# Kernel tuning notes

Hardware: AMD Instinct MI355X
Metric: run time of the kernel (lower is better)

## Reference

```python
import jax, jax.numpy as jnp
import numpy as np

N = 5000          # nodes (pool_ratios = [2000/5000, 0.5])
KS = (2000, 1000, 500)  # top-k sizes per level, depth=3
H = 128           # inter_dim
IN = 3            # xyz
OUT = 6890        # SMPL template vertices
E = 80000


def _gcn(adj, x, W, b):
    # GCNConv: add self-loops (weight 1), symmetric normalization
    n = adj.shape[0]
    A = adj + jnp.eye(n, dtype=adj.dtype)
    dinv = jax.lax.rsqrt(A.sum(axis=1))
    Ahat = dinv[:, None] * A * dinv[None, :]
    return Ahat @ (x @ W) + b


def _augment(adj):
    # GraphUNet.augment_adj: remove self loops, add self loops, A @ A, remove self loops
    n = adj.shape[0]
    eye = jnp.eye(n, dtype=adj.dtype)
    A = adj * (1.0 - eye) + eye
    A2 = A @ A
    return A2 * (1.0 - eye)


def _pool(x, adj, w, k):
    # TopKPooling: score = tanh(x.w / ||w||), keep top-k, scale kept features by score
    score = jnp.tanh((x @ w) / jnp.linalg.norm(w))
    sc, perm = jax.lax.top_k(score, k)
    x = x[perm] * sc[:, None]
    adj = adj[perm][:, perm]
    return x, adj, perm


def reference(pos, edge_index, Wd0, bd0, Wd1, bd1, Wd2, bd2, Wd3, bd3,
              pw0, pw1, pw2, Wu0, bu0, Wu1, bu1, Wu2, bu2,
              W1, b1, W2, b2, W3, b3):
    # eval mode: dropout_adj(p=0.1, training=False) is identity
    adj = jnp.zeros((N, N), pos.dtype).at[edge_index[0], edge_index[1]].add(1.0)

    x = jax.nn.relu(_gcn(adj, pos, Wd0, bd0))
    xs, adjs, perms = [x], [adj], []
    Wds = [(Wd1, bd1), (Wd2, bd2), (Wd3, bd3)]
    pws = [pw0, pw1, pw2]

    adj_cur = adj
    for i in range(3):
        a = _augment(adj_cur)
        x, adj_cur, perm = _pool(x, a, pws[i], KS[i])
        Wi, bi = Wds[i]
        x = jax.nn.relu(_gcn(adj_cur, x, Wi, bi))
        if i < 2:
            xs.append(x)
            adjs.append(adj_cur)
        perms.append(perm)

    Wus = [(Wu0, bu0), (Wu1, bu1), (Wu2, bu2)]
    for i in range(3):
        j = 2 - i
        res = xs[j]
        up = jnp.zeros_like(res).at[perms[j]].set(x)  # unpool: scatter back
        x = res + up                                   # sum_res=True
        Wi, bi = Wus[i]
        x = _gcn(adjs[j], x, Wi, bi)
        if i < 2:
            x = jax.nn.relu(x)

    x = x @ W1 + b1
    x = jax.nn.relu(x) @ W2 + b2
    x = x @ W3 + b3
    return jax.nn.log_softmax(x, axis=1)


def _glorot(k, shape):
    return (jax.random.normal(k, shape) * np.sqrt(2.0 / (shape[0] + shape[1]))).astype(jnp.float32)


def setup_inputs() -> dict:
    key = jax.random.key(0)
    ks = jax.random.split(key, 16)
    inp = {
        'pos': jax.random.normal(ks[0], (N, IN), dtype=jnp.float32),
        'edge_index': jax.random.randint(ks[1], (2, E), 0, N, dtype=jnp.int64),
        'Wd0': _glorot(ks[2], (IN, H)), 'bd0': jnp.zeros((H,), jnp.float32),
        'Wd1': _glorot(ks[3], (H, H)), 'bd1': jnp.zeros((H,), jnp.float32),
        'Wd2': _glorot(ks[4], (H, H)), 'bd2': jnp.zeros((H,), jnp.float32),
        'Wd3': _glorot(ks[5], (H, H)), 'bd3': jnp.zeros((H,), jnp.float32),
        'pw0': jax.random.normal(ks[6], (H,), dtype=jnp.float32) / np.sqrt(H),
        'pw1': jax.random.normal(ks[7], (H,), dtype=jnp.float32) / np.sqrt(H),
        'pw2': jax.random.normal(ks[8], (H,), dtype=jnp.float32) / np.sqrt(H),
        'Wu0': _glorot(ks[9], (H, H)), 'bu0': jnp.zeros((H,), jnp.float32),
        'Wu1': _glorot(ks[10], (H, H)), 'bu1': jnp.zeros((H,), jnp.float32),
        'Wu2': _glorot(ks[11], (H, H)), 'bu2': jnp.zeros((H,), jnp.float32),
        'W1': _glorot(ks[12], (H, H)), 'b1': jnp.zeros((H,), jnp.float32),
        'W2': _glorot(ks[13], (H, H)), 'b2': jnp.zeros((H,), jnp.float32),
        'W3': _glorot(ks[14], (H, OUT)), 'b3': jnp.zeros((OUT,), jnp.float32),
    }
    return inp
```

## Files before the change

### kernel.cpp

```cpp
#include <hip/hip_runtime.h>
#include <cmath>

#define CDIV(a,b) (((a)+(b)-1)/(b))

using u16 = unsigned short;
using short8 = __attribute__((ext_vector_type(8))) short;
using f32x4 = __attribute__((ext_vector_type(4))) float;

__device__ __forceinline__ u16 f2b(float v) {
    union { float f; unsigned u; } x; x.f = v;
    unsigned r = x.u + 0x7fffu + ((x.u >> 16) & 1u);
    return (u16)(r >> 16);
}
__device__ __forceinline__ float b2f(u16 h) {
    union { unsigned u; float f; } x; x.u = ((unsigned)h) << 16;
    return x.f;
}

#if defined(__has_builtin)
#if __has_builtin(__builtin_amdgcn_global_load_lds)
#define HAS_GLL 1
#endif
#endif
#ifndef HAS_GLL
#define HAS_GLL 0
#endif

__device__ __forceinline__ void g2l(const u16* g, uint4* l) {
#if HAS_GLL
    __builtin_amdgcn_global_load_lds((const __attribute__((address_space(1))) void*)g,
                                     (__attribute__((address_space(3))) void*)l, 16, 0, 0);
#else
    *l = *(const uint4*)g;
#endif
}


__global__ void build_adj_k(const int* __restrict__ ei, float* __restrict__ adj, int E, int ld) {
    int e = blockIdx.x * 256 + threadIdx.x;
    if (e < E) {
        int s = ei[e];
        int d = ei[E + e];
        atomicAdd(&adj[(size_t)s * ld + d], 1.0f);
    }
}

__global__ void rowsum_dinv_b_k(const u16* __restrict__ adjb, int ld, int n, float* __restrict__ dinv) {
    int i = blockIdx.x;
    __shared__ float red[256];
    const u16* row = adjb + (size_t)i * ld;
    float s = 0.f;
    for (int j = threadIdx.x; j < n; j += 256) s += b2f(row[j]);
    red[threadIdx.x] = s; __syncthreads();
    for (int w = 128; w > 0; w >>= 1) {
        if (threadIdx.x < w) red[threadIdx.x] += red[threadIdx.x + w];
        __syncthreads();
    }
    if (threadIdx.x == 0) dinv[i] = rsqrtf(red[0] + 1.0f);
}

__global__ void convS_k(const float* __restrict__ in, u16* __restrict__ out, size_t n4) {
    size_t i = (size_t)blockIdx.x * 256 + threadIdx.x;
    if (i < n4) {
        float4 v = ((const float4*)in)[i];
        ushort4 o;
        o.x = f2b(v.x); o.y = f2b(v.y); o.z = f2b(v.z); o.w = f2b(v.w);
        ((ushort4*)out)[i] = o;
    }
}

__global__ void transpose_b_k(const u16* __restrict__ in, u16* __restrict__ out, int n) {
    __shared__ u16 t[64][65];
    int i0 = blockIdx.y * 64, j0 = blockIdx.x * 64;
    for (int e = threadIdx.x; e < 4096; e += 256) {
        int r = e >> 6, c = e & 63;
        t[r][c] = in[(size_t)(i0 + r) * n + j0 + c];
    }
    __syncthreads();
    for (int e = threadIdx.x; e < 4096; e += 256) {
        int r = e >> 6, c = e & 63;
        out[(size_t)(j0 + r) * n + i0 + c] = t[c][r];
    }
}


__global__ void csr_cnt_k(const int* __restrict__ ei, int E, int* __restrict__ rowcnt) {
    int e = blockIdx.x * 256 + threadIdx.x;
    if (e < E) {
        int u = ei[e], v = ei[E + e];
        if (u != v) atomicAdd(&rowcnt[u], 1);
    }
}

__global__ __launch_bounds__(1024) void prefix_k(const int* __restrict__ cnt, int* __restrict__ ptr, int n) {
    __shared__ int buf[5120];
    for (int i = threadIdx.x; i < 5120; i += 1024) buf[i] = (i < n) ? cnt[i] : 0;
    __syncthreads();
    for (int d = 1; d < 5120; d <<= 1) {
        int vals[5];
#pragma unroll
        for (int c = 0; c < 5; ++c) {
            int i = threadIdx.x + c * 1024;
            vals[c] = (i >= d) ? buf[i - d] : 0;
        }
        __syncthreads();
#pragma unroll
        for (int c = 0; c < 5; ++c) {
            int i = threadIdx.x + c * 1024;
            buf[i] += vals[c];
        }
        __syncthreads();
    }
    for (int i = threadIdx.x; i <= n; i += 1024) ptr[i] = (i == 0) ? 0 : buf[i - 1];
}

__global__ void csr_fill_k(const int* __restrict__ ei, int E, const int* __restrict__ rowptr,
                           int* __restrict__ fill, int* __restrict__ cols) {
    int e = blockIdx.x * 256 + threadIdx.x;
    if (e < E) {
        int u = ei[e], v = ei[E + e];
        if (u != v) {
            int p = rowptr[u] + atomicAdd(&fill[u], 1);
            cols[p] = v;
        }
    }
}

__global__ void inv_k(const int* __restrict__ perm, int k, int* __restrict__ inv) {
    int r = blockIdx.x * 256 + threadIdx.x;
    if (r < k) inv[perm[r]] = r;
}

__global__ __launch_bounds__(256) void spgemm_k(const int* __restrict__ perm, const int* __restrict__ rowptr,
                                                const int* __restrict__ cols, const int* __restrict__ inv,
                                                int* __restrict__ A2, int ldo) {
    __shared__ int nb[256];
    __shared__ int degs;
    int a = blockIdx.x;
    int pa = perm[a];
    int s = rowptr[pa], epos = rowptr[pa + 1];
    int d = epos - s;
    if (threadIdx.x == 0) degs = d > 256 ? 256 : d;
    if (threadIdx.x < d && threadIdx.x < 256) nb[threadIdx.x] = cols[s + threadIdx.x];
    __syncthreads();
    int* rowA2 = A2 + (size_t)a * ldo;
    for (int p = s + threadIdx.x; p < epos; p += 256) {
        int b = inv[cols[p]];
        if (b >= 0) atomicAdd(&rowA2[b], 2);
    }
    int dd = degs;
    for (int j = 0; j < dd; ++j) {
        int kk = nb[j];
        int s2 = rowptr[kk], e2 = rowptr[kk + 1];
        for (int p = s2 + threadIdx.x; p < e2; p += 256) {
            int b = inv[cols[p]];
            if (b >= 0) atomicAdd(&rowA2[b], 1);
        }
    }
}

__global__ void conv_spg_k(const int* __restrict__ A2, int kNew, int Mp, u16* __restrict__ out) {
    int r = blockIdx.x;
    for (int j = threadIdx.x; j < Mp; j += 256) {
        int v = 0;
        if (r < kNew && j < kNew && j != r) v = A2[(size_t)r * Mp + j];
        out[(size_t)r * Mp + j] = f2b((float)v);
    }
}


template<int SA, int SB>
__global__ __launch_bounds__(256) void mm_nt(const u16* __restrict__ A0, const u16* __restrict__ A1,
                                             const u16* __restrict__ B0, const u16* __restrict__ B1,
                                             float* __restrict__ C, const float* __restrict__ cbias,
                                             int M, int N, int lda, int ldb, int ldc,
                                             int kPerZ, int Kpad, size_t cstride) {
    __shared__ uint4 lds_t[(2 + SA + SB) * 512];
    uint4* Ab  = lds_t;
    uint4* A1b = lds_t + (SA ? 512 : 0);
    uint4* Bb  = lds_t + (1 + SA) * 512;
    uint4* B1b = Bb + (SB ? 512 : 0);

    int tid = threadIdx.x;

    int nx = gridDim.x, nxy = nx * gridDim.y;
    int bx = blockIdx.x, by = blockIdx.y;
    if ((nxy & 7) == 0) {
        int flat = by * nx + bx;
        int nf = (flat & 7) * (nxy >> 3) + (flat >> 3);
        bx = nf % nx; by = nf / nx;
    }
    int row0 = by * 128, col0 = bx * 128;

    int kbeg = blockIdx.z * kPerZ;
    int kend = min(kbeg + kPerZ, Kpad);
    C += (size_t)blockIdx.z * cstride;

    int wave = tid >> 6, lane = tid & 63;
    int wr = (wave >> 1) * 64, wc = (wave & 1) * 64;
    int lrow = lane & 15, kg = lane >> 4;

    int tS0 = tid, tS1 = tid + 256;
    int R0 = ((tS0 >> 6) << 4) | (tS0 & 15), kc0 = (tS0 >> 4) & 3;
    int R1 = ((tS1 >> 6) << 4) | (tS1 & 15), kc1 = (tS1 >> 4) & 3;

    const u16* aP0 = A0 + (size_t)(row0 + R0) * lda + kbeg + kc0 * 8;
    const u16* aP1 = A0 + (size_t)(row0 + R1) * lda + kbeg + kc1 * 8;
    const u16* bP0 = B0 + (size_t)(col0 + R0) * ldb + kbeg + kc0 * 8;
    const u16* bP1 = B0 + (size_t)(col0 + R1) * ldb + kbeg + kc1 * 8;
    const u16* a1P0 = SA ? (A1 + (size_t)(row0 + R0) * lda + kbeg + kc0 * 8) : nullptr;
    const u16* a1P1 = SA ? (A1 + (size_t)(row0 + R1) * lda + kbeg + kc1 * 8) : nullptr;
    const u16* b1P0 = SB ? (B1 + (size_t)(col0 + R0) * ldb + kbeg + kc0 * 8) : nullptr;
    const u16* b1P1 = SB ? (B1 + (size_t)(col0 + R1) * ldb + kbeg + kc1 * 8) : nullptr;

    f32x4 acc[4][4] = {};

    for (int k0 = kbeg; k0 < kend; k0 += 32) {
        __syncthreads();
        g2l(aP0, Ab + tS0);
        g2l(aP1, Ab + tS1);
        if constexpr (SA) { g2l(a1P0, A1b + tS0); g2l(a1P1, A1b + tS1); }
        g2l(bP0, Bb + tS0);
        g2l(bP1, Bb + tS1);
        if constexpr (SB) { g2l(b1P0, B1b + tS0); g2l(b1P1, B1b + tS1); }
        __syncthreads();

        const short8* Ap  = (const short8*)Ab;
        const short8* A1p = (const short8*)A1b;
        const short8* Bp  = (const short8*)Bb;
        const short8* B1p = (const short8*)B1b;

        short8 a[4], a1[4], b[4], b1[4];
#pragma unroll
        for (int m = 0; m < 4; ++m) {
            int idx = (((wr >> 4) + m) << 6) | (kg << 4) | lrow;
            a[m] = Ap[idx];
            if constexpr (SA) a1[m] = A1p[idx];
        }
#pragma unroll
        for (int n = 0; n < 4; ++n) {
            int idx = (((wc >> 4) + n) << 6) | (kg << 4) | lrow;
            b[n] = Bp[idx];
            if constexpr (SB) b1[n] = B1p[idx];
        }
#pragma unroll
        for (int m = 0; m < 4; ++m)
#pragma unroll
            for (int n = 0; n < 4; ++n) {
                acc[m][n] = __builtin_amdgcn_mfma_f32_16x16x32_bf16(a[m], b[n], acc[m][n], 0, 0, 0);
                if constexpr (SA) acc[m][n] = __builtin_amdgcn_mfma_f32_16x16x32_bf16(a1[m], b[n], acc[m][n], 0, 0, 0);
                if constexpr (SB) acc[m][n] = __builtin_amdgcn_mfma_f32_16x16x32_bf16(a[m], b1[n], acc[m][n], 0, 0, 0);
            }

        aP0 += 32; aP1 += 32; bP0 += 32; bP1 += 32;
        if constexpr (SA) { a1P0 += 32; a1P1 += 32; }
        if constexpr (SB) { b1P0 += 32; b1P1 += 32; }
    }

#pragma unroll
    for (int m = 0; m < 4; ++m) {
        int rm = row0 + wr + m * 16 + kg * 4;
#pragma unroll
        for (int n = 0; n < 4; ++n) {
            int cc = col0 + wc + n * 16 + lrow;
            if (cc >= N) continue;
            float badd = cbias ? cbias[cc] : 0.f;
#pragma unroll
            for (int i = 0; i < 4; ++i) {
                int r = rm + i;
                if (r < M) C[(size_t)r * ldc + cc] = acc[m][n][i] + badd;
            }
        }
    }
}


__global__ __launch_bounds__(256) void gemm64(const float* __restrict__ A, const float* __restrict__ B,
                                              float* __restrict__ C,
                                              int M, int N, int K, int lda, int ldb, int ldc,
                                              const float* __restrict__ bias, int relu) {
    __shared__ float As[16][65];
    __shared__ float Bs[16][65];
    int tid = threadIdx.x;
    int trow = tid / 16, tcol = tid % 16;
    int row0 = blockIdx.y * 64 + trow * 4;
    int col0 = blockIdx.x * 64 + tcol * 4;
    float acc[4][4] = {};
    int am = tid >> 2;
    int ak = (tid & 3) * 4;
    int bk = tid >> 4;
    int bn = (tid & 15) * 4;
    for (int k0 = 0; k0 < K; k0 += 16) {
        int gm = blockIdx.y * 64 + am;
#pragma unroll
        for (int u = 0; u < 4; ++u) {
            int gk = k0 + ak + u;
            As[ak + u][am] = (gm < M && gk < K) ? A[(size_t)gm * lda + gk] : 0.f;
        }
        int gbk = k0 + bk;
#pragma unroll
        for (int u = 0; u < 4; ++u) {
            int gn = blockIdx.x * 64 + bn + u;
            Bs[bk][bn + u] = (gbk < K && gn < N) ? B[(size_t)gbk * ldb + gn] : 0.f;
        }
        __syncthreads();
#pragma unroll
        for (int kk = 0; kk < 16; ++kk) {
            float a[4], b[4];
#pragma unroll
            for (int i = 0; i < 4; ++i) a[i] = As[kk][trow * 4 + i];
#pragma unroll
            for (int j = 0; j < 4; ++j) b[j] = Bs[kk][tcol * 4 + j];
#pragma unroll
            for (int i = 0; i < 4; ++i)
#pragma unroll
                for (int j = 0; j < 4; ++j) acc[i][j] += a[i] * b[j];
        }
        __syncthreads();
    }
#pragma unroll
    for (int i = 0; i < 4; ++i) {
        int r = row0 + i;
        if (r >= M) continue;
#pragma unroll
        for (int j = 0; j < 4; ++j) {
            int c = col0 + j;
            if (c < N) {
                float v = acc[i][j] + (bias ? bias[c] : 0.f);
                if (relu) v = fmaxf(v, 0.f);
                C[(size_t)r * ldc + c] = v;
            }
        }
    }
}


__global__ void scale_split_k(const float* __restrict__ xw, const float* __restrict__ dinv,
                              u16* __restrict__ zhT, u16* __restrict__ zlT, int M, int ldz) {
    __shared__ float t[32][33];
    int i0 = blockIdx.x * 32, f0 = blockIdx.y * 32;
#pragma unroll
    for (int it = 0; it < 4; ++it) {
        int r = it * 8 + (threadIdx.x >> 5);
        int c = threadIdx.x & 31;
        int i = i0 + r;
        t[r][c] = (i < M) ? dinv[i] * xw[(size_t)i * 128 + f0 + c] : 0.f;
    }
    __syncthreads();
#pragma unroll
    for (int it = 0; it < 4; ++it) {
        int r = it * 8 + (threadIdx.x >> 5);
        int c = threadIdx.x & 31;
        int f = f0 + r, i = i0 + c;
        float v = t[c][r];
        u16 h = f2b(v);
        zhT[(size_t)f * ldz + i] = h;
        zlT[(size_t)f * ldz + i] = f2b(v - b2f(h));
    }
}

__global__ void reduce_gcn_post_k(const float* __restrict__ part, int Z, int Mp,
                                  const float* __restrict__ xw, const float* __restrict__ dinv,
                                  const float* __restrict__ bias, float* __restrict__ y, int relu) {
    int i = blockIdx.x, f = threadIdx.x;
    size_t idx = (size_t)i * 128 + f;
    float s = 0.f;
    for (int z = 0; z < Z; ++z) s += part[(size_t)z * Mp * 128 + idx];
    float di = dinv[i];
    float v = di * s + di * di * xw[idx] + bias[f];
    y[idx] = relu ? fmaxf(v, 0.f) : v;
}


__global__ void score_k(const float* __restrict__ x, const float* __restrict__ pw,
                        float* __restrict__ score) {
    int i = blockIdx.x;
    __shared__ float red[128], red2[128];
    float p = pw[threadIdx.x];
    red[threadIdx.x]  = x[(size_t)i * 128 + threadIdx.x] * p;
    red2[threadIdx.x] = p * p;
    __syncthreads();
    for (int s = 64; s > 0; s >>= 1) {
        if (threadIdx.x < s) { red[threadIdx.x] += red[threadIdx.x + s]; red2[threadIdx.x] += red2[threadIdx.x + s]; }
        __syncthreads();
    }
    if (threadIdx.x == 0) score[i] = tanhf(red[0] / sqrtf(red2[0]));
}

__global__ __launch_bounds__(256) void rank_partial_k(const float* __restrict__ score, int n,
                                                      int* __restrict__ rankpart) {
    __shared__ float s_sh[512];
    int i = blockIdx.x * 256 + threadIdx.x;
    int jbase = blockIdx.y * 512;
    float si = (i < n) ? score[i] : -3.0f;
    for (int t = threadIdx.x; t < 512; t += 256) {
        int j = jbase + t;
        s_sh[t] = (j < n) ? score[j] : -3.0f;
    }
    __syncthreads();
    int cnt = 0;
#pragma unroll 16
    for (int t = 0; t < 512; ++t) {
        float sj = s_sh[t];
        cnt += (sj > si) || (sj == si && (jbase + t) < i);
    }
    if (i < n) rankpart[blockIdx.y * n + i] = cnt;
}

__global__ void scatter_topk_k(const float* __restrict__ score, const int* __restrict__ rankpart,
                               int nsl, int n, int k, int* __restrict__ perm, float* __restrict__ sc) {
    int i = blockIdx.x * 256 + threadIdx.x;
    if (i >= n) return;
    int r = 0;
    for (int s = 0; s < nsl; ++s) r += rankpart[s * n + i];
    if (r < k) { perm[r] = i; sc[r] = score[i]; }
}

__global__ void pool_x_k(float* __restrict__ xo, const float* __restrict__ xi,
                         const int* __restrict__ perm, const float* __restrict__ sc) {
    int a = blockIdx.x, f = threadIdx.x;
    xo[(size_t)a * 128 + f] = xi[(size_t)perm[a] * 128 + f] * sc[a];
}

__global__ void gather2_b_k(const u16* __restrict__ src0, const u16* __restrict__ src1,
                            int ldsrc, const int* __restrict__ perm,
                            u16* __restrict__ dst0, u16* __restrict__ dst1, int width) {
    const u16* src = blockIdx.y ? src1 : src0;
    u16* dst = blockIdx.y ? dst1 : dst0;
    int row = blockIdx.x;
    int p = perm[row];
    const uint4* s4 = (const uint4*)(src + (size_t)p * ldsrc);
    uint4* d4 = (uint4*)(dst + (size_t)row * width);
    int n8 = width >> 3;
    for (int j = threadIdx.x; j < n8; j += 256) d4[j] = s4[j];
    __syncthreads();
    if (threadIdx.x == 0) dst[(size_t)row * width + p] = 0x3F80;
}

__global__ void reduce_pool_k(const float* __restrict__ part, int Z, int k, int Mp, u16* __restrict__ out) {
    int row = blockIdx.x;
    for (int j = threadIdx.x; j < Mp; j += 256) {
        float s = 0.f;
        if (row < k && j < k) {
            for (int z = 0; z < Z; ++z) s += part[(size_t)z * Mp * Mp + (size_t)row * Mp + j];
            if (j == row) s = 0.f;
        }
        out[(size_t)row * Mp + j] = f2b(s);
    }
}

__global__ void scatter_add_k(float* __restrict__ xdst, const int* __restrict__ perm,
                              const float* __restrict__ xsrc) {
    int a = blockIdx.x, f = threadIdx.x;
    xdst[(size_t)perm[a] * 128 + f] += xsrc[(size_t)a * 128 + f];
}


__global__ void split_head_k(const float* __restrict__ x, u16* __restrict__ Ah, u16* __restrict__ Al) {
    int i = blockIdx.x, f = threadIdx.x;
    size_t idx = (size_t)i * 128 + f;
    float v = x[idx];
    u16 h = f2b(v);
    Ah[idx] = h;
    Al[idx] = f2b(v - b2f(h));
}

__global__ void convW3T_k(const float* __restrict__ W3, u16* __restrict__ W3T, int Nc, int Ncp) {
    __shared__ float t[64][65];
    int k0 = blockIdx.y * 64, n0 = blockIdx.x * 64;
    for (int e = threadIdx.x; e < 4096; e += 256) {
        int r = e >> 6, c = e & 63;
        t[r][c] = (k0 + r < 128 && n0 + c < Nc) ? W3[(size_t)(k0 + r) * Nc + n0 + c] : 0.f;
    }
    __syncthreads();
    for (int e = threadIdx.x; e < 4096; e += 256) {
        int r = e >> 6, c = e & 63;
        int nn = n0 + r, kk = k0 + c;
        if (nn < Ncp) W3T[(size_t)nn * 128 + kk] = f2b(t[c][r]);
    }
}

__global__ __launch_bounds__(256) void logsoftmax_k(float* __restrict__ out) {
    const int C = 6890;
    const int CPT = 27;
    int row = blockIdx.x;
    float* rowp = out + (size_t)row * C;
    __shared__ float red[256];

    float v[CPT];
    float mx = -1e30f;
#pragma unroll
    for (int u = 0; u < CPT; ++u) {
        int c = threadIdx.x + u * 256;
        v[u] = (c < C) ? rowp[c] : -1e30f;
        mx = fmaxf(mx, v[u]);
    }
    red[threadIdx.x] = mx; __syncthreads();
    for (int s = 128; s > 0; s >>= 1) {
        if (threadIdx.x < s) red[threadIdx.x] = fmaxf(red[threadIdx.x], red[threadIdx.x + s]);
        __syncthreads();
    }
    float m = red[0];
    __syncthreads();

    float sum = 0.f;
#pragma unroll
    for (int u = 0; u < CPT; ++u) sum += __expf(v[u] - m);
    red[threadIdx.x] = sum; __syncthreads();
    for (int s = 128; s > 0; s >>= 1) {
        if (threadIdx.x < s) red[threadIdx.x] += red[threadIdx.x + s];
        __syncthreads();
    }
    float ls = m + logf(red[0]);

#pragma unroll
    for (int u = 0; u < CPT; ++u) {
        int c = threadIdx.x + u * 256;
        if (c < C) rowp[c] = v[u] - ls;
    }
}


extern "C" void kernel_launch(void* const* d_in, const int* in_sizes, int n_in,
                              void* d_out, int out_size, void* d_ws, size_t ws_size,
                              hipStream_t stream) {
    const int N0 = 5000, K1 = 2000, K2 = 1000, K3 = 500, E = 80000, OUTC = 6890;
    const int Np0 = 5120, Kp1 = 2048, Kp2 = 1024, Kp3 = 512, OUTCP = 6912;
    (void)in_sizes; (void)n_in; (void)out_size; (void)ws_size;

    const float* pos = (const float*)d_in[0];
    const int*   ei  = (const int*)d_in[1];
    const float* Wd0 = (const float*)d_in[2];  const float* bd0 = (const float*)d_in[3];
    const float* Wd1 = (const float*)d_in[4];  const float* bd1 = (const float*)d_in[5];
    const float* Wd2 = (const float*)d_in[6];  const float* bd2 = (const float*)d_in[7];
    const float* Wd3 = (const float*)d_in[8];  const float* bd3 = (const float*)d_in[9];
    const float* pw0 = (const float*)d_in[10];
    const float* pw1 = (const float*)d_in[11];
    const float* pw2 = (const float*)d_in[12];
    const float* Wu0 = (const float*)d_in[13]; const float* bu0 = (const float*)d_in[14];
    const float* Wu1 = (const float*)d_in[15]; const float* bu1 = (const float*)d_in[16];
    const float* Wu2 = (const float*)d_in[17]; const float* bu2 = (const float*)d_in[18];
    const float* W1  = (const float*)d_in[19]; const float* b1  = (const float*)d_in[20];
    const float* W2  = (const float*)d_in[21]; const float* b2  = (const float*)d_in[22];
    const float* W3  = (const float*)d_in[23]; const float* b3  = (const float*)d_in[24];

    float* w = (float*)d_ws;
    size_t off = 0;
    auto alloc = [&](size_t nel) { float* p = w + off; off += nel; return p; };

    float* pool = alloc(26220000);
    float* adj0 = pool;
    float* partials = pool;
    u16* G   = (u16*)(pool + 13000000);
    u16* HT  = (u16*)(pool + 18250000);
    u16* zhT = (u16*)(pool + 13000000);
    u16* zlT = (u16*)(pool + 13400000);
    u16* Ah  = (u16*)(pool);
    u16* Al  = (u16*)(pool + 400000);

    u16* adj0b  = (u16*)alloc(13107200);
    u16* adj1b  = (u16*)alloc(2097152);
    u16* adj1bT = (u16*)alloc(2097152);
    u16* adj2b  = (u16*)alloc(524288);
    u16* adj2bT = (u16*)alloc(524288);
    u16* adj3b  = (u16*)alloc(131072);
    u16* W3T    = (u16*)alloc(442368);

    float* x0 = alloc((size_t)N0 * 128);
    float* x1 = alloc((size_t)K1 * 128);
    float* x2 = alloc((size_t)K2 * 128);
    float* xa = alloc((size_t)N0 * 128);
    float* xb = alloc((size_t)N0 * 128);
    float* xw = alloc((size_t)N0 * 128);
    float* dinv0 = alloc(N0); float* dinv1 = alloc(K1); float* dinv2 = alloc(K2); float* dinv3 = alloc(K3);
    float* scorev = alloc(N0);
    float* scv    = alloc(K1);
    int* perm0 = (int*)alloc(K1);
    int* perm1 = (int*)alloc(K2);
    int* perm2 = (int*)alloc(K3);
    int* rankpart = (int*)alloc(50048);
    int* rowcnt = (int*)alloc(5120);
    int* rowptr = (int*)alloc(5120);
    int* fillc  = (int*)alloc(5120);
    int* colsb  = (int*)alloc(80000);
    int* invb   = (int*)alloc(5120);

    auto launch_mm = [&](int SA, int SB, const u16* A0, const u16* A1, const u16* B0, const u16* B1,
                         float* Cc, const float* cbias, int M, int N, int Kpad,
                         int lda, int ldb, int ldc, size_t cstride, int Z) -> int {
        int kPerZ = CDIV(Kpad, Z * 32) * 32;
        int gz = CDIV(Kpad, kPerZ);
        dim3 g(CDIV(N, 128), CDIV(M, 128), gz);
        if (SA)      mm_nt<1, 0><<<g, 256, 0, stream>>>(A0, A1, B0, B1, Cc, cbias, M, N, lda, ldb, ldc, kPerZ, Kpad, cstride);
        else if (SB) mm_nt<0, 1><<<g, 256, 0, stream>>>(A0, A1, B0, B1, Cc, cbias, M, N, lda, ldb, ldc, kPerZ, Kpad, cstride);
        else         mm_nt<0, 0><<<g, 256, 0, stream>>>(A0, A1, B0, B1, Cc, cbias, M, N, lda, ldb, ldc, kPerZ, Kpad, cstride);
        return gz;
    };

    auto run_gcn = [&](const u16* adjb, int n, int Np,
                       const float* x, int kin, const float* W, const float* bias,
                       const float* dinv, int relu, float* y, int Z) {
        gemm64<<<dim3(2, CDIV(n, 64)), 256, 0, stream>>>(x, W, xw, n, 128, kin, kin, 128, 128, nullptr, 0);
        scale_split_k<<<dim3(Np / 32, 4), 256, 0, stream>>>(xw, dinv, zhT, zlT, n, Np);
        int gz = launch_mm(0, 1, adjb, nullptr, zhT, zlT, partials, nullptr,
                           Np, 128, Np, Np, Np, 128, (size_t)Np * 128, Z);
        reduce_gcn_post_k<<<n, 128, 0, stream>>>(partials, gz, Np, xw, dinv, bias, y, relu);
    };

    auto run_pool = [&](const float* x, int n, int Np, int kNew, int KpNew, const float* pw,
                        const u16* srcb, const u16* srcbT, u16* adjNew, int* perm, int Z) {
        score_k<<<n, 128, 0, stream>>>(x, pw, scorev);
        int nsl = CDIV(n, 512);
        rank_partial_k<<<dim3(CDIV(n, 256), nsl), 256, 0, stream>>>(scorev, n, rankpart);
        scatter_topk_k<<<CDIV(n, 256), 256, 0, stream>>>(scorev, rankpart, nsl, n, kNew, perm, scv);
        pool_x_k<<<kNew, 128, 0, stream>>>(xa, x, perm, scv);
        gather2_b_k<<<dim3(kNew, 2), 256, 0, stream>>>(srcb, srcbT, Np, perm, G, HT, Np);
        int gz = launch_mm(0, 0, G, nullptr, HT, nullptr, partials, nullptr,
                           KpNew, KpNew, Np, Np, Np, KpNew, (size_t)KpNew * KpNew, Z);
        reduce_pool_k<<<KpNew, 256, 0, stream>>>(partials, gz, kNew, KpNew, adjNew);
    };

    hipMemsetAsync(adj0, 0, (size_t)Np0 * Np0 * sizeof(float), stream);
    hipMemsetAsync(rowcnt, 0, N0 * sizeof(int), stream);
    hipMemsetAsync(fillc, 0, N0 * sizeof(int), stream);
    build_adj_k<<<CDIV(E, 256), 256, 0, stream>>>(ei, adj0, E, Np0);
    csr_cnt_k<<<CDIV(E, 256), 256, 0, stream>>>(ei, E, rowcnt);
    prefix_k<<<1, 1024, 0, stream>>>(rowcnt, rowptr, N0);
    csr_fill_k<<<CDIV(E, 256), 256, 0, stream>>>(ei, E, rowptr, fillc, colsb);
    convS_k<<<CDIV((size_t)Np0 * Np0 / 4, 256), 256, 0, stream>>>(adj0, adj0b, (size_t)Np0 * Np0 / 4);
    rowsum_dinv_b_k<<<N0, 256, 0, stream>>>(adj0b, Np0, Np0, dinv0);

    run_gcn(adj0b, N0, Np0, pos, 3, Wd0, bd0, dinv0, 1, x0, 10);

    score_k<<<N0, 128, 0, stream>>>(x0, pw0, scorev);
    {
        int nsl = CDIV(N0, 512);
        rank_partial_k<<<dim3(CDIV(N0, 256), nsl), 256, 0, stream>>>(scorev, N0, rankpart);
        scatter_topk_k<<<CDIV(N0, 256), 256, 0, stream>>>(scorev, rankpart, nsl, N0, K1, perm0, scv);
    }
    pool_x_k<<<K1, 128, 0, stream>>>(xa, x0, perm0, scv);
    hipMemsetAsync(invb, 0xFF, N0 * sizeof(int), stream);
    inv_k<<<CDIV(K1, 256), 256, 0, stream>>>(perm0, K1, invb);
    int* A2i = (int*)partials;
    hipMemsetAsync(A2i, 0, (size_t)Kp1 * Kp1 * sizeof(int), stream);
    spgemm_k<<<K1, 256, 0, stream>>>(perm0, rowptr, colsb, invb, A2i, Kp1);
    conv_spg_k<<<Kp1, 256, 0, stream>>>(A2i, K1, Kp1, adj1b);

    transpose_b_k<<<dim3(Kp1 / 64, Kp1 / 64), 256, 0, stream>>>(adj1b, adj1bT, Kp1);
    rowsum_dinv_b_k<<<K1, 256, 0, stream>>>(adj1b, Kp1, Kp1, dinv1);
    run_gcn(adj1b, K1, Kp1, xa, 128, Wd1, bd1, dinv1, 1, x1, 16);

    run_pool(x1, K1, Kp1, K2, Kp2, pw1, adj1b, adj1bT, adj2b, perm1, 8);
    transpose_b_k<<<dim3(Kp2 / 64, Kp2 / 64), 256, 0, stream>>>(adj2b, adj2bT, Kp2);
    rowsum_dinv_b_k<<<K2, 256, 0, stream>>>(adj2b, Kp2, Kp2, dinv2);
    run_gcn(adj2b, K2, Kp2, xa, 128, Wd2, bd2, dinv2, 1, x2, 16);

    run_pool(x2, K2, Kp2, K3, Kp3, pw2, adj2b, adj2bT, adj3b, perm2, 8);
    rowsum_dinv_b_k<<<K3, 256, 0, stream>>>(adj3b, Kp3, Kp3, dinv3);
    run_gcn(adj3b, K3, Kp3, xa, 128, Wd3, bd3, dinv3, 1, xb, 8);

    hipMemcpyAsync(xa, x2, (size_t)K2 * 128 * sizeof(float), hipMemcpyDeviceToDevice, stream);
    scatter_add_k<<<K3, 128, 0, stream>>>(xa, perm2, xb);
    run_gcn(adj2b, K2, Kp2, xa, 128, Wu0, bu0, dinv2, 1, xb, 16);

    hipMemcpyAsync(xa, x1, (size_t)K1 * 128 * sizeof(float), hipMemcpyDeviceToDevice, stream);
    scatter_add_k<<<K2, 128, 0, stream>>>(xa, perm1, xb);
    run_gcn(adj1b, K1, Kp1, xa, 128, Wu1, bu1, dinv1, 1, xb, 16);

    hipMemcpyAsync(xa, x0, (size_t)N0 * 128 * sizeof(float), hipMemcpyDeviceToDevice, stream);
    scatter_add_k<<<K1, 128, 0, stream>>>(xa, perm0, xb);
    run_gcn(adj0b, N0, Np0, xa, 128, Wu2, bu2, dinv0, 0, xb, 10);

    gemm64<<<dim3(2, CDIV(N0, 64)), 256, 0, stream>>>(xb, W1, xa, N0, 128, 128, 128, 128, 128, b1, 1);
    gemm64<<<dim3(2, CDIV(N0, 64)), 256, 0, stream>>>(xa, W2, xw, N0, 128, 128, 128, 128, 128, b2, 0);

    split_head_k<<<N0, 128, 0, stream>>>(xw, Ah, Al);
    convW3T_k<<<dim3(OUTCP / 64, 2), 256, 0, stream>>>(W3, W3T, OUTC, OUTCP);

    float* outp = (float*)d_out;
    launch_mm(1, 0, Ah, Al, W3T, nullptr, outp, b3, N0, OUTC, 128, 128, 128, OUTC, 0, 1);
    logsoftmax_k<<<N0, 256, 0, stream>>>(outp);
}
```

Measured before the change: 817.1 us.

## Replace dense level-0 adjacency GCN with sorted CSR sparse SpMM

Drops the dense 5120x5120 adjacency build, its bf16 conversion, the dense row-sum and the dense GEMM for the two level-0 GCN layers. Those now run as a CSR SpMM with degrees taken from the edge counts. Self-loop edges are now kept in the CSR and skipped inside the SpGEMM instead. Rows are insertion-sorted so the fp32 summation order is deterministic. This removes large memory traffic and a big dense matmul, in exchange for serial per-row sorting and a simple one-block-per-row SpMM.

```diff
diff --git a/kernel.cpp b/kernel.cpp
--- a/kernel.cpp
+++ b/kernel.cpp
@@ -36,60 +36,9 @@
 }
 
 
-__global__ void build_adj_k(const int* __restrict__ ei, float* __restrict__ adj, int E, int ld) {
-    int e = blockIdx.x * 256 + threadIdx.x;
-    if (e < E) {
-        int s = ei[e];
-        int d = ei[E + e];
-        atomicAdd(&adj[(size_t)s * ld + d], 1.0f);
-    }
-}
-
-__global__ void rowsum_dinv_b_k(const u16* __restrict__ adjb, int ld, int n, float* __restrict__ dinv) {
-    int i = blockIdx.x;
-    __shared__ float red[256];
-    const u16* row = adjb + (size_t)i * ld;
-    float s = 0.f;
-    for (int j = threadIdx.x; j < n; j += 256) s += b2f(row[j]);
-    red[threadIdx.x] = s; __syncthreads();
-    for (int w = 128; w > 0; w >>= 1) {
-        if (threadIdx.x < w) red[threadIdx.x] += red[threadIdx.x + w];
-        __syncthreads();
-    }
-    if (threadIdx.x == 0) dinv[i] = rsqrtf(red[0] + 1.0f);
-}
-
-__global__ void convS_k(const float* __restrict__ in, u16* __restrict__ out, size_t n4) {
-    size_t i = (size_t)blockIdx.x * 256 + threadIdx.x;
-    if (i < n4) {
-        float4 v = ((const float4*)in)[i];
-        ushort4 o;
-        o.x = f2b(v.x); o.y = f2b(v.y); o.z = f2b(v.z); o.w = f2b(v.w);
-        ((ushort4*)out)[i] = o;
-    }
-}
-
-__global__ void transpose_b_k(const u16* __restrict__ in, u16* __restrict__ out, int n) {
-    __shared__ u16 t[64][65];
-    int i0 = blockIdx.y * 64, j0 = blockIdx.x * 64;
-    for (int e = threadIdx.x; e < 4096; e += 256) {
-        int r = e >> 6, c = e & 63;
-        t[r][c] = in[(size_t)(i0 + r) * n + j0 + c];
-    }
-    __syncthreads();
-    for (int e = threadIdx.x; e < 4096; e += 256) {
-        int r = e >> 6, c = e & 63;
-        out[(size_t)(j0 + r) * n + i0 + c] = t[c][r];
-    }
-}
-
-
 __global__ void csr_cnt_k(const int* __restrict__ ei, int E, int* __restrict__ rowcnt) {
     int e = blockIdx.x * 256 + threadIdx.x;
-    if (e < E) {
-        int u = ei[e], v = ei[E + e];
-        if (u != v) atomicAdd(&rowcnt[u], 1);
-    }
+    if (e < E) atomicAdd(&rowcnt[ei[e]], 1);
 }
 
 __global__ __launch_bounds__(1024) void prefix_k(const int* __restrict__ cnt, int* __restrict__ ptr, int n) {
@@ -118,13 +67,44 @@
                            int* __restrict__ fill, int* __restrict__ cols) {
     int e = blockIdx.x * 256 + threadIdx.x;
     if (e < E) {
-        int u = ei[e], v = ei[E + e];
-        if (u != v) {
-            int p = rowptr[u] + atomicAdd(&fill[u], 1);
-            cols[p] = v;
-        }
-    }
-}
+        int u = ei[e];
+        int p = rowptr[u] + atomicAdd(&fill[u], 1);
+        cols[p] = ei[E + e];
+    }
+}
+
+__global__ void sortrows_k(const int* __restrict__ rowptr, int* __restrict__ cols, int n) {
+    int i = blockIdx.x * 256 + threadIdx.x;
+    if (i >= n) return;
+    int s = rowptr[i], e = rowptr[i + 1];
+    for (int p = s + 1; p < e; ++p) {
+        int v = cols[p];
+        int q = p - 1;
+        while (q >= s && cols[q] > v) { cols[q + 1] = cols[q]; --q; }
+        cols[q + 1] = v;
+    }
+}
+
+__global__ void dinv_from_cnt_k(const int* __restrict__ cnt, float* __restrict__ dinv, int n) {
+    int i = blockIdx.x * 256 + threadIdx.x;
+    if (i < n) dinv[i] = rsqrtf((float)cnt[i] + 1.0f);
+}
+
+__global__ __launch_bounds__(128) void spmm_gcn_k(const int* __restrict__ rowptr, const int* __restrict__ cols,
+                                                  const float* __restrict__ dinv, const float* __restrict__ xw,
+                                                  const float* __restrict__ bias, float* __restrict__ y, int relu) {
+    int i = blockIdx.x, f = threadIdx.x;
+    int s = rowptr[i], e = rowptr[i + 1];
+    float acc = 0.f;
+    for (int p = s; p < e; ++p) {
+        int d = cols[p];
+        acc += dinv[d] * xw[(size_t)d * 128 + f];
+    }
+    float di = dinv[i];
+    float v = di * acc + di * di * xw[(size_t)i * 128 + f] + bias[f];
+    y[(size_t)i * 128 + f] = relu ? fmaxf(v, 0.f) : v;
+}
+
 
 __global__ void inv_k(const int* __restrict__ perm, int k, int* __restrict__ inv) {
     int r = blockIdx.x * 256 + threadIdx.x;
@@ -145,16 +125,23 @@
     __syncthreads();
     int* rowA2 = A2 + (size_t)a * ldo;
     for (int p = s + threadIdx.x; p < epos; p += 256) {
-        int b = inv[cols[p]];
-        if (b >= 0) atomicAdd(&rowA2[b], 2);
+        int c = cols[p];
+        if (c != pa) {
+            int b = inv[c];
+            if (b >= 0) atomicAdd(&rowA2[b], 2);
+        }
     }
     int dd = degs;
     for (int j = 0; j < dd; ++j) {
         int kk = nb[j];
+        if (kk == pa) continue;
         int s2 = rowptr[kk], e2 = rowptr[kk + 1];
         for (int p = s2 + threadIdx.x; p < e2; p += 256) {
-            int b = inv[cols[p]];
-            if (b >= 0) atomicAdd(&rowA2[b], 1);
+            int pb = cols[p];
+            if (pb != kk) {
+                int b = inv[pb];
+                if (b >= 0) atomicAdd(&rowA2[b], 1);
+            }
         }
     }
 }
@@ -165,6 +152,35 @@
         int v = 0;
         if (r < kNew && j < kNew && j != r) v = A2[(size_t)r * Mp + j];
         out[(size_t)r * Mp + j] = f2b((float)v);
+    }
+}
+
+
+__global__ void rowsum_dinv_b_k(const u16* __restrict__ adjb, int ld, int n, float* __restrict__ dinv) {
+    int i = blockIdx.x;
+    __shared__ float red[256];
+    const u16* row = adjb + (size_t)i * ld;
+    float s = 0.f;
+    for (int j = threadIdx.x; j < n; j += 256) s += b2f(row[j]);
+    red[threadIdx.x] = s; __syncthreads();
+    for (int w = 128; w > 0; w >>= 1) {
+        if (threadIdx.x < w) red[threadIdx.x] += red[threadIdx.x + w];
+        __syncthreads();
+    }
+    if (threadIdx.x == 0) dinv[i] = rsqrtf(red[0] + 1.0f);
+}
+
+__global__ void transpose_b_k(const u16* __restrict__ in, u16* __restrict__ out, int n) {
+    __shared__ u16 t[64][65];
+    int i0 = blockIdx.y * 64, j0 = blockIdx.x * 64;
+    for (int e = threadIdx.x; e < 4096; e += 256) {
+        int r = e >> 6, c = e & 63;
+        t[r][c] = in[(size_t)(i0 + r) * n + j0 + c];
+    }
+    __syncthreads();
+    for (int e = threadIdx.x; e < 4096; e += 256) {
+        int r = e >> 6, c = e & 63;
+        out[(size_t)(j0 + r) * n + i0 + c] = t[c][r];
     }
 }
 
@@ -525,7 +541,7 @@
                               void* d_out, int out_size, void* d_ws, size_t ws_size,
                               hipStream_t stream) {
     const int N0 = 5000, K1 = 2000, K2 = 1000, K3 = 500, E = 80000, OUTC = 6890;
-    const int Np0 = 5120, Kp1 = 2048, Kp2 = 1024, Kp3 = 512, OUTCP = 6912;
+    const int Kp1 = 2048, Kp2 = 1024, Kp3 = 512, OUTCP = 6912;
     (void)in_sizes; (void)n_in; (void)out_size; (void)ws_size;
 
     const float* pos = (const float*)d_in[0];
@@ -549,7 +565,6 @@
     auto alloc = [&](size_t nel) { float* p = w + off; off += nel; return p; };
 
     float* pool = alloc(26220000);
-    float* adj0 = pool;
     float* partials = pool;
     u16* G   = (u16*)(pool + 13000000);
     u16* HT  = (u16*)(pool + 18250000);
@@ -558,7 +573,6 @@
     u16* Ah  = (u16*)(pool);
     u16* Al  = (u16*)(pool + 400000);
 
-    u16* adj0b  = (u16*)alloc(13107200);
     u16* adj1b  = (u16*)alloc(2097152);
     u16* adj1bT = (u16*)alloc(2097152);
     u16* adj2b  = (u16*)alloc(524288);
@@ -598,13 +612,18 @@
     };
 
     auto run_gcn = [&](const u16* adjb, int n, int Np,
-                       const float* x, int kin, const float* W, const float* bias,
+                       const float* x, const float* W, const float* bias,
                        const float* dinv, int relu, float* y, int Z) {
-        gemm64<<<dim3(2, CDIV(n, 64)), 256, 0, stream>>>(x, W, xw, n, 128, kin, kin, 128, 128, nullptr, 0);
+        gemm64<<<dim3(2, CDIV(n, 64)), 256, 0, stream>>>(x, W, xw, n, 128, 128, 128, 128, 128, nullptr, 0);
         scale_split_k<<<dim3(Np / 32, 4), 256, 0, stream>>>(xw, dinv, zhT, zlT, n, Np);
         int gz = launch_mm(0, 1, adjb, nullptr, zhT, zlT, partials, nullptr,
                            Np, 128, Np, Np, Np, 128, (size_t)Np * 128, Z);
         reduce_gcn_post_k<<<n, 128, 0, stream>>>(partials, gz, Np, xw, dinv, bias, y, relu);
+    };
+
+    auto run_gcn_sp = [&](const float* x, int kin, const float* W, const float* bias, int relu, float* y) {
+        gemm64<<<dim3(2, CDIV(N0, 64)), 256, 0, stream>>>(x, W, xw, N0, 128, kin, kin, 128, 128, nullptr, 0);
+        spmm_gcn_k<<<N0, 128, 0, stream>>>(rowptr, colsb, dinv0, xw, bias, y, relu);
     };
 
     auto run_pool = [&](const float* x, int n, int Np, int kNew, int KpNew, const float* pw,
@@ -620,17 +639,15 @@
         reduce_pool_k<<<KpNew, 256, 0, stream>>>(partials, gz, kNew, KpNew, adjNew);
     };
 
-    hipMemsetAsync(adj0, 0, (size_t)Np0 * Np0 * sizeof(float), stream);
     hipMemsetAsync(rowcnt, 0, N0 * sizeof(int), stream);
     hipMemsetAsync(fillc, 0, N0 * sizeof(int), stream);
-    build_adj_k<<<CDIV(E, 256), 256, 0, stream>>>(ei, adj0, E, Np0);
     csr_cnt_k<<<CDIV(E, 256), 256, 0, stream>>>(ei, E, rowcnt);
     prefix_k<<<1, 1024, 0, stream>>>(rowcnt, rowptr, N0);
     csr_fill_k<<<CDIV(E, 256), 256, 0, stream>>>(ei, E, rowptr, fillc, colsb);
-    convS_k<<<CDIV((size_t)Np0 * Np0 / 4, 256), 256, 0, stream>>>(adj0, adj0b, (size_t)Np0 * Np0 / 4);
-    rowsum_dinv_b_k<<<N0, 256, 0, stream>>>(adj0b, Np0, Np0, dinv0);
-
-    run_gcn(adj0b, N0, Np0, pos, 3, Wd0, bd0, dinv0, 1, x0, 10);
+    sortrows_k<<<CDIV(N0, 256), 256, 0, stream>>>(rowptr, colsb, N0);
+    dinv_from_cnt_k<<<CDIV(N0, 256), 256, 0, stream>>>(rowcnt, dinv0, N0);
+
+    run_gcn_sp(pos, 3, Wd0, bd0, 1, x0);
 
     score_k<<<N0, 128, 0, stream>>>(x0, pw0, scorev);
     {
@@ -648,28 +665,28 @@
 
     transpose_b_k<<<dim3(Kp1 / 64, Kp1 / 64), 256, 0, stream>>>(adj1b, adj1bT, Kp1);
     rowsum_dinv_b_k<<<K1, 256, 0, stream>>>(adj1b, Kp1, Kp1, dinv1);
-    run_gcn(adj1b, K1, Kp1, xa, 128, Wd1, bd1, dinv1, 1, x1, 16);
+    run_gcn(adj1b, K1, Kp1, xa, Wd1, bd1, dinv1, 1, x1, 16);
 
     run_pool(x1, K1, Kp1, K2, Kp2, pw1, adj1b, adj1bT, adj2b, perm1, 8);
     transpose_b_k<<<dim3(Kp2 / 64, Kp2 / 64), 256, 0, stream>>>(adj2b, adj2bT, Kp2);
     rowsum_dinv_b_k<<<K2, 256, 0, stream>>>(adj2b, Kp2, Kp2, dinv2);
-    run_gcn(adj2b, K2, Kp2, xa, 128, Wd2, bd2, dinv2, 1, x2, 16);
+    run_gcn(adj2b, K2, Kp2, xa, Wd2, bd2, dinv2, 1, x2, 16);
 
     run_pool(x2, K2, Kp2, K3, Kp3, pw2, adj2b, adj2bT, adj3b, perm2, 8);
     rowsum_dinv_b_k<<<K3, 256, 0, stream>>>(adj3b, Kp3, Kp3, dinv3);
-    run_gcn(adj3b, K3, Kp3, xa, 128, Wd3, bd3, dinv3, 1, xb, 8);
+    run_gcn(adj3b, K3, Kp3, xa, Wd3, bd3, dinv3, 1, xb, 8);
 
     hipMemcpyAsync(xa, x2, (size_t)K2 * 128 * sizeof(float), hipMemcpyDeviceToDevice, stream);
     scatter_add_k<<<K3, 128, 0, stream>>>(xa, perm2, xb);
-    run_gcn(adj2b, K2, Kp2, xa, 128, Wu0, bu0, dinv2, 1, xb, 16);
+    run_gcn(adj2b, K2, Kp2, xa, Wu0, bu0, dinv2, 1, xb, 16);
 
     hipMemcpyAsync(xa, x1, (size_t)K1 * 128 * sizeof(float), hipMemcpyDeviceToDevice, stream);
     scatter_add_k<<<K2, 128, 0, stream>>>(xa, perm1, xb);
-    run_gcn(adj1b, K1, Kp1, xa, 128, Wu1, bu1, dinv1, 1, xb, 16);
+    run_gcn(adj1b, K1, Kp1, xa, Wu1, bu1, dinv1, 1, xb, 16);
 
     hipMemcpyAsync(xa, x0, (size_t)N0 * 128 * sizeof(float), hipMemcpyDeviceToDevice, stream);
     scatter_add_k<<<K1, 128, 0, stream>>>(xa, perm0, xb);
-    run_gcn(adj0b, N0, Np0, xa, 128, Wu2, bu2, dinv0, 0, xb, 10);
+    run_gcn_sp(xa, 128, Wu2, bu2, 0, xb);
 
     gemm64<<<dim3(2, CDIV(N0, 64)), 256, 0, stream>>>(xb, W1, xa, N0, 128, 128, 128, 128, 128, b1, 1);
     gemm64<<<dim3(2, CDIV(N0, 64)), 256, 0, stream>>>(xa, W2, xw, N0, 128, 128, 128, 128, 128, b2, 0);
```

Measured after the change: 725.9 us. -11.2%, faster.
